# Performance work log

Hardware: AMD Instinct MI355X
Metric: run time of the kernel (lower is better)

Reference implementation:

```python
import jax, jax.numpy as jnp
import numpy as np

KV_SIZE = 512


def setup_inputs() -> dict:
    key = jax.random.key(0)
    k1, k2, k3 = jax.random.split(key, 3)
    B, T, C = 8, 4096, 1024
    x = jax.random.normal(k1, (B, T, C), dtype=jnp.float32)
    k_t_1 = jax.random.normal(k2, (B, KV_SIZE, C), dtype=jnp.float32)
    v_t_1 = jax.random.normal(k3, (B, KV_SIZE, C), dtype=jnp.float32)
    return {"x": x, "k_t_1": k_t_1, "v_t_1": v_t_1}


def reference(x, k_t_1, v_t_1):
    # x: [B, T, C]; latent state k_t_1, v_t_1: [B, S=512, C]
    B, T, C = x.shape
    scale = 1.0 / jnp.sqrt(jnp.asarray(C, dtype=x.dtype))

    # Read: queries (tokens) attend over the fixed-size latent KV state.
    scores = jnp.einsum("btc,bsc->bts", x, k_t_1) * scale      # [B, T, S]
    att = jnp.einsum("bts,bsc->btc", jax.nn.softmax(scores, axis=-1), v_t_1)

    # Update: each latent slot attends over the incoming tokens and
    # accumulates the summary into the state (fixed-size KV cache update).
    k_scores = jnp.einsum("bsc,btc->bst", k_t_1, x) * scale     # [B, S, T]
    k_t = k_t_1 + jnp.einsum("bst,btc->bsc", jax.nn.softmax(k_scores, axis=-1), x)
    v_scores = jnp.einsum("bsc,btc->bst", v_t_1, x) * scale     # [B, S, T]
    v_t = v_t_1 + jnp.einsum("bst,btc->bsc", jax.nn.softmax(v_scores, axis=-1), x)

    return att, k_t, v_t
```

## Files before the change

kernel.cpp:

```cpp
#include <hip/hip_runtime.h>
#include <hip/hip_bf16.h>

#define BB 8
#define TT 4096
#define CC 1024
#define SS 512

typedef __bf16 bf16x8 __attribute__((ext_vector_type(8)));
typedef float f32x4 __attribute__((ext_vector_type(4)));
typedef unsigned short u16x8 __attribute__((ext_vector_type(8)));

__device__ __forceinline__ float bf2f(unsigned short u) {
  union { unsigned int i; float f; } x; x.i = ((unsigned int)u) << 16; return x.f;
}
__device__ __forceinline__ unsigned short f2bf(float f) {
  __hip_bfloat16 h = __float2bfloat16(f);
  unsigned short u; __builtin_memcpy(&u, &h, 2); return u;
}

__global__ void cvt_transpose(const float* __restrict__ in,
                              unsigned short* __restrict__ out_rm,
                              unsigned short* __restrict__ out_t,
                              int R, int Cd) {
  __shared__ float tile[64][65];
  const long bo = (long)blockIdx.z * R * Cd;
  const int r0 = blockIdx.x * 64, c0 = blockIdx.y * 64;
  const int tx = threadIdx.x, ty = threadIdx.y;
#pragma unroll
  for (int i = 0; i < 16; ++i) {
    int r = ty + i * 4;
    float v = in[bo + (long)(r0 + r) * Cd + c0 + tx];
    tile[r][tx] = v;
    out_rm[bo + (long)(r0 + r) * Cd + c0 + tx] = f2bf(v);
  }
  if (out_t != nullptr) {
    __syncthreads();
#pragma unroll
    for (int i = 0; i < 16; ++i) {
      int c = ty + i * 4;
      out_t[bo + (long)(c0 + c) * R + r0 + tx] = f2bf(tile[tx][c]);
    }
  }
}

__global__ void transpose_bf16(const unsigned short* __restrict__ in,
                               unsigned short* __restrict__ out,
                               int Rin, int Cin) {
  __shared__ unsigned short tile[64][72];
  const long bo = (long)blockIdx.z * Rin * Cin;
  const int r0 = blockIdx.x * 64, c0 = blockIdx.y * 64;
  const int tid = threadIdx.x;
  const int lr = tid >> 3;
  const int lc = (tid & 7) * 8;
#pragma unroll
  for (int p = 0; p < 2; ++p) {
    int r = lr + p * 32;
    *(u16x8*)&tile[r][lc] = *(const u16x8*)&in[bo + (long)(r0 + r) * Cin + c0 + lc];
  }
  __syncthreads();
#pragma unroll
  for (int p = 0; p < 2; ++p) {
    int s = lr + p * 32;
    u16x8 val;
#pragma unroll
    for (int j = 0; j < 8; ++j) val[j] = tile[lc + j][s];
    *(u16x8*)&out[bo + (long)(c0 + s) * Rin + r0 + lc] = val;
  }
}

template <int ROWLEN>
__global__ __launch_bounds__(256) void row_softmax(unsigned short* __restrict__ sc) {
  constexpr int NV = ROWLEN / 512;
  const int lane = threadIdx.x & 63;
  const long row = (long)blockIdx.x * 4 + (threadIdx.x >> 6);
  unsigned short* base = sc + row * (long)ROWLEN;
  u16x8 d[NV];
  float m = -1e30f;
#pragma unroll
  for (int v = 0; v < NV; ++v) {
    d[v] = *(const u16x8*)&base[(v * 64 + lane) * 8];
#pragma unroll
    for (int j = 0; j < 8; ++j) m = fmaxf(m, bf2f(d[v][j]));
  }
#pragma unroll
  for (int off = 32; off >= 1; off >>= 1) m = fmaxf(m, __shfl_xor(m, off, 64));
  float l = 0.f;
#pragma unroll
  for (int v = 0; v < NV; ++v) {
#pragma unroll
    for (int j = 0; j < 8; ++j) {
      float e = __expf(bf2f(d[v][j]) - m);
      l += e;
      d[v][j] = f2bf(e);
    }
  }
#pragma unroll
  for (int off = 32; off >= 1; off >>= 1) l += __shfl_xor(l, off, 64);
  const float inv = 1.f / l;
#pragma unroll
  for (int v = 0; v < NV; ++v) {
    u16x8 o;
#pragma unroll
    for (int j = 0; j < 8; ++j) o[j] = f2bf(bf2f(d[v][j]) * inv);
    *(u16x8*)&base[(v * 64 + lane) * 8] = o;
  }
}

template <bool OUT_BF16, bool RESID>
__global__ __launch_bounds__(256) void gemm_bt(
    const unsigned short* __restrict__ A, int lda, long sA,
    const unsigned short* __restrict__ Bt, int ldb, long sB,
    void* __restrict__ Cout, int ldc, long sC,
    const float* __restrict__ resid, long sR,
    float alpha, int M, int N, int K) {
  __shared__ unsigned short As[128 * 64];
  __shared__ unsigned short Bs[128 * 64];
  const int zb = blockIdx.z;
  const unsigned short* Ab = A + (long)zb * sA;
  const unsigned short* Bb = Bt + (long)zb * sB;
  const int m0 = blockIdx.y * 128;
  const int n0 = blockIdx.x * 128;
  const int tid = threadIdx.x;
  const int lane = tid & 63;
  const int wm = (tid >> 6) & 1;
  const int wn = tid >> 7;
  const int srow = tid >> 3;
  const int scol = (tid & 7) * 8;
  f32x4 zero = {0.f, 0.f, 0.f, 0.f};
  f32x4 acc[4][4];
#pragma unroll
  for (int i = 0; i < 4; ++i)
#pragma unroll
    for (int j = 0; j < 4; ++j) acc[i][j] = zero;

  for (int k0 = 0; k0 < K; k0 += 64) {
#pragma unroll
    for (int p = 0; p < 4; ++p) {
      int r = srow + p * 32;
      const unsigned short* g = Ab + (long)(m0 + r) * lda + k0 + scol;
      __builtin_amdgcn_global_load_lds(
          (const __attribute__((address_space(1))) void*)g,
          (__attribute__((address_space(3))) void*)&As[r * 64 + scol], 16, 0, 0);
    }
#pragma unroll
    for (int p = 0; p < 4; ++p) {
      int r = srow + p * 32;
      const unsigned short* g = Bb + (long)(n0 + r) * ldb + k0 + scol;
      __builtin_amdgcn_global_load_lds(
          (const __attribute__((address_space(1))) void*)g,
          (__attribute__((address_space(3))) void*)&Bs[r * 64 + scol], 16, 0, 0);
    }
    __syncthreads();
#pragma unroll
    for (int kk = 0; kk < 2; ++kk) {
      const int kof = kk * 32 + (lane >> 4) * 8;
      bf16x8 af[4], bfr[4];
#pragma unroll
      for (int i = 0; i < 4; ++i)
        af[i] = *(const bf16x8*)&As[(wm * 64 + i * 16 + (lane & 15)) * 64 + kof];
#pragma unroll
      for (int j = 0; j < 4; ++j)
        bfr[j] = *(const bf16x8*)&Bs[(wn * 64 + j * 16 + (lane & 15)) * 64 + kof];
#pragma unroll
      for (int i = 0; i < 4; ++i)
#pragma unroll
        for (int j = 0; j < 4; ++j)
          acc[i][j] = __builtin_amdgcn_mfma_f32_16x16x32_bf16(af[i], bfr[j], acc[i][j], 0, 0, 0);
    }
    __syncthreads();
  }
  const int rbase = (lane >> 4) * 4;
  const int cl = lane & 15;
#pragma unroll
  for (int i = 0; i < 4; ++i)
#pragma unroll
    for (int j = 0; j < 4; ++j)
#pragma unroll
      for (int r = 0; r < 4; ++r) {
        int row = m0 + wm * 64 + i * 16 + rbase + r;
        int col = n0 + wn * 64 + j * 16 + cl;
        long idx = (long)row * ldc + col;
        float v = acc[i][j][r] * alpha;
        if (RESID) v += resid[(long)zb * sR + idx];
        if (OUT_BF16)
          ((unsigned short*)Cout)[(long)zb * sC + idx] = f2bf(v);
        else
          ((float*)Cout)[(long)zb * sC + idx] = v;
      }
}

extern "C" void kernel_launch(void* const* d_in, const int* in_sizes, int n_in,
                              void* d_out, int out_size, void* d_ws, size_t ws_size,
                              hipStream_t stream) {
  const float* x = (const float*)d_in[0];
  const float* kin = (const float*)d_in[1];
  const float* vin = (const float*)d_in[2];

  float* att = (float*)d_out;
  float* kt = att + (long)BB * TT * CC;
  float* vt = kt + (long)BB * SS * CC;

  unsigned short* xb = (unsigned short*)d_out;
  unsigned short* xT = xb + (long)BB * TT * CC;

  char* w = (char*)d_ws;
  unsigned short* kb = (unsigned short*)w; w += (long)BB * SS * CC * 2;
  unsigned short* vb = (unsigned short*)w; w += (long)BB * SS * CC * 2;
  unsigned short* vT = (unsigned short*)w; w += (long)BB * CC * SS * 2;
  unsigned short* sc = (unsigned short*)w; w += (long)BB * TT * SS * 2;
  unsigned short* pk = (unsigned short*)w; w += (long)BB * SS * TT * 2;

  const float scale = 0.03125f;
  dim3 cblk(64, 4);

  cvt_transpose<<<dim3(TT / 64, CC / 64, BB), cblk, 0, stream>>>(x, xb, xT, TT, CC);
  cvt_transpose<<<dim3(SS / 64, CC / 64, BB), cblk, 0, stream>>>(kin, kb, (unsigned short*)nullptr, SS, CC);
  cvt_transpose<<<dim3(SS / 64, CC / 64, BB), cblk, 0, stream>>>(vin, vb, vT, SS, CC);

  gemm_bt<true, false><<<dim3(SS / 128, TT / 128, BB), 256, 0, stream>>>(
      xb, CC, (long)TT * CC, kb, CC, (long)SS * CC, sc, SS, (long)TT * SS,
      nullptr, 0, scale, TT, SS, CC);

  transpose_bf16<<<dim3(TT / 64, SS / 64, BB), 256, 0, stream>>>(sc, pk, TT, SS);
  row_softmax<TT><<<BB * SS / 4, 256, 0, stream>>>(pk);

  gemm_bt<false, true><<<dim3(CC / 128, SS / 128, BB), 256, 0, stream>>>(
      pk, TT, (long)SS * TT, xT, TT, (long)CC * TT, kt, CC, (long)SS * CC,
      kin, (long)SS * CC, 1.f, SS, CC, TT);

  row_softmax<SS><<<BB * TT / 4, 256, 0, stream>>>(sc);

  gemm_bt<true, false><<<dim3(TT / 128, SS / 128, BB), 256, 0, stream>>>(
      vb, CC, (long)SS * CC, xb, CC, (long)TT * CC, pk, TT, (long)SS * TT,
      nullptr, 0, scale, SS, TT, CC);
  row_softmax<TT><<<BB * SS / 4, 256, 0, stream>>>(pk);

  gemm_bt<false, true><<<dim3(CC / 128, SS / 128, BB), 256, 0, stream>>>(
      pk, TT, (long)SS * TT, xT, TT, (long)CC * TT, vt, CC, (long)SS * CC,
      vin, (long)SS * CC, 1.f, SS, CC, TT);

  gemm_bt<false, false><<<dim3(CC / 128, TT / 128, BB), 256, 0, stream>>>(
      sc, SS, (long)TT * SS, vT, SS, (long)CC * SS, att, CC, (long)TT * CC,
      nullptr, 0, 1.f, TT, CC, SS);
}
```

Before: 717.3 us.

## Split-K the update GEMMs with atomics and batch the K/V score GEMMs

The P·x update GEMMs now split their long T reduction across extra blocks and accumulate with float atomics. The k_t/v_t outputs are pre-seeded with the fp32 inputs during conversion, so the residual add is folded in. When the workspace is large enough, the K and V score GEMMs run as one launch over stacked rows, and their softmaxes also run as one launch. The T×S score matrix for the read path is obtained by transposing the k·xᵀ scores instead of recomputing them. This targets under-occupancy of the 256-block update GEMMs, at the cost of atomic traffic, nondeterministic summation order, and workspace aliasing that depends on ws_size.

Result: faster. 700.2 us (-2.4%).

```diff
diff --git a/kernel.cpp b/kernel.cpp
--- a/kernel.cpp
+++ b/kernel.cpp
@@ -21,6 +21,7 @@
 __global__ void cvt_transpose(const float* __restrict__ in,
                               unsigned short* __restrict__ out_rm,
                               unsigned short* __restrict__ out_t,
+                              float* __restrict__ out_f32,
                               int R, int Cd) {
   __shared__ float tile[64][65];
   const long bo = (long)blockIdx.z * R * Cd;
@@ -32,6 +33,7 @@
     float v = in[bo + (long)(r0 + r) * Cd + c0 + tx];
     tile[r][tx] = v;
     out_rm[bo + (long)(r0 + r) * Cd + c0 + tx] = f2bf(v);
+    if (out_f32 != nullptr) out_f32[bo + (long)(r0 + r) * Cd + c0 + tx] = v;
   }
   if (out_t != nullptr) {
     __syncthreads();
@@ -45,9 +47,10 @@
 
 __global__ void transpose_bf16(const unsigned short* __restrict__ in,
                                unsigned short* __restrict__ out,
-                               int Rin, int Cin) {
+                               int Rin, int Cin, long sIn, long sOut) {
   __shared__ unsigned short tile[64][72];
-  const long bo = (long)blockIdx.z * Rin * Cin;
+  const long bi = (long)blockIdx.z * sIn;
+  const long bo = (long)blockIdx.z * sOut;
   const int r0 = blockIdx.x * 64, c0 = blockIdx.y * 64;
   const int tid = threadIdx.x;
   const int lr = tid >> 3;
@@ -55,7 +58,7 @@
 #pragma unroll
   for (int p = 0; p < 2; ++p) {
     int r = lr + p * 32;
-    *(u16x8*)&tile[r][lc] = *(const u16x8*)&in[bo + (long)(r0 + r) * Cin + c0 + lc];
+    *(u16x8*)&tile[r][lc] = *(const u16x8*)&in[bi + (long)(r0 + r) * Cin + c0 + lc];
   }
   __syncthreads();
 #pragma unroll
@@ -106,19 +109,27 @@
   }
 }
 
-template <bool OUT_BF16, bool RESID>
+template <bool OUT_BF16, bool ATOMIC>
 __global__ __launch_bounds__(256) void gemm_bt(
-    const unsigned short* __restrict__ A, int lda, long sA,
+    const unsigned short* __restrict__ A,
+    const unsigned short* __restrict__ A2, int lda, long sA,
     const unsigned short* __restrict__ Bt, int ldb, long sB,
-    void* __restrict__ Cout, int ldc, long sC,
-    const float* __restrict__ resid, long sR,
-    float alpha, int M, int N, int K) {
+    void* __restrict__ Cout, void* __restrict__ Cout2, int ldc, long sC,
+    float alpha, int M, int N, int K, int halfM, int kshift) {
   __shared__ unsigned short As[128 * 64];
   __shared__ unsigned short Bs[128 * 64];
-  const int zb = blockIdx.z;
-  const unsigned short* Ab = A + (long)zb * sA;
+  const int zb = blockIdx.z >> kshift;
+  const int kch = blockIdx.z & ((1 << kshift) - 1);
+  const int Kc = K >> kshift;
+  const int kstart = kch * Kc;
+  const int kend = kstart + Kc;
+  const int m0full = blockIdx.y * 128;
+  const bool hi = m0full >= halfM;
+  const unsigned short* Ab = ((hi && A2 != nullptr) ? A2 : A) + (long)zb * sA;
+  const int mA = (hi && A2 != nullptr) ? m0full - halfM : m0full;
+  void* Cbase = (hi && Cout2 != nullptr) ? Cout2 : Cout;
+  const int mC = (hi && Cout2 != nullptr) ? m0full - halfM : m0full;
   const unsigned short* Bb = Bt + (long)zb * sB;
-  const int m0 = blockIdx.y * 128;
   const int n0 = blockIdx.x * 128;
   const int tid = threadIdx.x;
   const int lane = tid & 63;
@@ -133,11 +144,11 @@
 #pragma unroll
     for (int j = 0; j < 4; ++j) acc[i][j] = zero;
 
-  for (int k0 = 0; k0 < K; k0 += 64) {
+  for (int k0 = kstart; k0 < kend; k0 += 64) {
 #pragma unroll
     for (int p = 0; p < 4; ++p) {
       int r = srow + p * 32;
-      const unsigned short* g = Ab + (long)(m0 + r) * lda + k0 + scol;
+      const unsigned short* g = Ab + (long)(mA + r) * lda + k0 + scol;
       __builtin_amdgcn_global_load_lds(
           (const __attribute__((address_space(1))) void*)g,
           (__attribute__((address_space(3))) void*)&As[r * 64 + scol], 16, 0, 0);
@@ -177,15 +188,17 @@
     for (int j = 0; j < 4; ++j)
 #pragma unroll
       for (int r = 0; r < 4; ++r) {
-        int row = m0 + wm * 64 + i * 16 + rbase + r;
+        int row = mC + wm * 64 + i * 16 + rbase + r;
         int col = n0 + wn * 64 + j * 16 + cl;
-        long idx = (long)row * ldc + col;
+        long idx = (long)zb * sC + (long)row * ldc + col;
         float v = acc[i][j][r] * alpha;
-        if (RESID) v += resid[(long)zb * sR + idx];
-        if (OUT_BF16)
-          ((unsigned short*)Cout)[(long)zb * sC + idx] = f2bf(v);
-        else
-          ((float*)Cout)[(long)zb * sC + idx] = v;
+        if (ATOMIC) {
+          unsafeAtomicAdd(&((float*)Cbase)[idx], v);
+        } else if (OUT_BF16) {
+          ((unsigned short*)Cbase)[idx] = f2bf(v);
+        } else {
+          ((float*)Cbase)[idx] = v;
+        }
       }
 }
 
@@ -203,43 +216,73 @@
   unsigned short* xb = (unsigned short*)d_out;
   unsigned short* xT = xb + (long)BB * TT * CC;
 
-  char* w = (char*)d_ws;
-  unsigned short* kb = (unsigned short*)w; w += (long)BB * SS * CC * 2;
-  unsigned short* vb = (unsigned short*)w; w += (long)BB * SS * CC * 2;
-  unsigned short* vT = (unsigned short*)w; w += (long)BB * CC * SS * 2;
-  unsigned short* sc = (unsigned short*)w; w += (long)BB * TT * SS * 2;
-  unsigned short* pk = (unsigned short*)w; w += (long)BB * SS * TT * 2;
-
   const float scale = 0.03125f;
   dim3 cblk(64, 4);
-
-  cvt_transpose<<<dim3(TT / 64, CC / 64, BB), cblk, 0, stream>>>(x, xb, xT, TT, CC);
-  cvt_transpose<<<dim3(SS / 64, CC / 64, BB), cblk, 0, stream>>>(kin, kb, (unsigned short*)nullptr, SS, CC);
-  cvt_transpose<<<dim3(SS / 64, CC / 64, BB), cblk, 0, stream>>>(vin, vb, vT, SS, CC);
-
-  gemm_bt<true, false><<<dim3(SS / 128, TT / 128, BB), 256, 0, stream>>>(
-      xb, CC, (long)TT * CC, kb, CC, (long)SS * CC, sc, SS, (long)TT * SS,
-      nullptr, 0, scale, TT, SS, CC);
-
-  transpose_bf16<<<dim3(TT / 64, SS / 64, BB), 256, 0, stream>>>(sc, pk, TT, SS);
-  row_softmax<TT><<<BB * SS / 4, 256, 0, stream>>>(pk);
-
-  gemm_bt<false, true><<<dim3(CC / 128, SS / 128, BB), 256, 0, stream>>>(
-      pk, TT, (long)SS * TT, xT, TT, (long)CC * TT, kt, CC, (long)SS * CC,
-      kin, (long)SS * CC, 1.f, SS, CC, TT);
-
-  row_softmax<SS><<<BB * TT / 4, 256, 0, stream>>>(sc);
-
-  gemm_bt<true, false><<<dim3(TT / 128, SS / 128, BB), 256, 0, stream>>>(
-      vb, CC, (long)SS * CC, xb, CC, (long)TT * CC, pk, TT, (long)SS * TT,
-      nullptr, 0, scale, SS, TT, CC);
-  row_softmax<TT><<<BB * SS / 4, 256, 0, stream>>>(pk);
-
-  gemm_bt<false, true><<<dim3(CC / 128, SS / 128, BB), 256, 0, stream>>>(
-      pk, TT, (long)SS * TT, xT, TT, (long)CC * TT, vt, CC, (long)SS * CC,
-      vin, (long)SS * CC, 1.f, SS, CC, TT);
-
-  gemm_bt<false, false><<<dim3(CC / 128, TT / 128, BB), 256, 0, stream>>>(
-      sc, SS, (long)TT * SS, vT, SS, (long)CC * SS, att, CC, (long)TT * CC,
-      nullptr, 0, 1.f, TT, CC, SS);
-}
+  const long MiB = 1024 * 1024;
+
+  if (ws_size >= (size_t)(104 * MiB)) {
+    char* w = (char*)d_ws;
+    unsigned short* sc  = (unsigned short*)w;
+    unsigned short* kb  = (unsigned short*)w;
+    unsigned short* vb  = (unsigned short*)(w + 8 * MiB);
+    unsigned short* vT  = (unsigned short*)(w + 32 * MiB);
+    unsigned short* pkv = (unsigned short*)(w + 40 * MiB);
+
+    cvt_transpose<<<dim3(TT / 64, CC / 64, BB), cblk, 0, stream>>>(x, xb, xT, nullptr, TT, CC);
+    cvt_transpose<<<dim3(SS / 64, CC / 64, BB), cblk, 0, stream>>>(kin, kb, nullptr, kt, SS, CC);
+    cvt_transpose<<<dim3(SS / 64, CC / 64, BB), cblk, 0, stream>>>(vin, vb, vT, vt, SS, CC);
+
+    gemm_bt<true, false><<<dim3(TT / 128, 2 * SS / 128, BB), 256, 0, stream>>>(
+        kb, vb, CC, (long)SS * CC, xb, CC, (long)TT * CC,
+        pkv, nullptr, TT, (long)2 * SS * TT, scale, 2 * SS, TT, CC, SS, 0);
+
+    transpose_bf16<<<dim3(SS / 64, TT / 64, BB), 256, 0, stream>>>(
+        pkv, sc, SS, TT, (long)2 * SS * TT, (long)TT * SS);
+
+    row_softmax<TT><<<BB * 2 * SS / 4, 256, 0, stream>>>(pkv);
+
+    gemm_bt<false, true><<<dim3(CC / 128, 2 * SS / 128, BB * 2), 256, 0, stream>>>(
+        pkv, nullptr, TT, (long)2 * SS * TT, xT, TT, (long)CC * TT,
+        kt, vt, CC, (long)SS * CC, 1.f, 2 * SS, CC, TT, SS, 1);
+
+    row_softmax<SS><<<BB * TT / 4, 256, 0, stream>>>(sc);
+
+    gemm_bt<false, false><<<dim3(CC / 128, TT / 128, BB), 256, 0, stream>>>(
+        sc, nullptr, SS, (long)TT * SS, vT, SS, (long)CC * SS,
+        att, nullptr, CC, (long)TT * CC, 1.f, TT, CC, SS, 1 << 30, 0);
+  } else {
+    char* w = (char*)d_ws;
+    unsigned short* kb = (unsigned short*)w;
+    unsigned short* vb = (unsigned short*)(w + 8 * MiB);
+    unsigned short* vT = (unsigned short*)(w + 16 * MiB);
+    unsigned short* sc = (unsigned short*)(w + 24 * MiB);
+    unsigned short* pk = (unsigned short*)(w + 56 * MiB);
+
+    cvt_transpose<<<dim3(TT / 64, CC / 64, BB), cblk, 0, stream>>>(x, xb, xT, nullptr, TT, CC);
+    cvt_transpose<<<dim3(SS / 64, CC / 64, BB), cblk, 0, stream>>>(kin, kb, nullptr, kt, SS, CC);
+    cvt_transpose<<<dim3(SS / 64, CC / 64, BB), cblk, 0, stream>>>(vin, vb, vT, vt, SS, CC);
+
+    gemm_bt<true, false><<<dim3(TT / 128, SS / 128, BB), 256, 0, stream>>>(
+        kb, nullptr, CC, (long)SS * CC, xb, CC, (long)TT * CC,
+        pk, nullptr, TT, (long)SS * TT, scale, SS, TT, CC, 1 << 30, 0);
+    transpose_bf16<<<dim3(SS / 64, TT / 64, BB), 256, 0, stream>>>(
+        pk, sc, SS, TT, (long)SS * TT, (long)TT * SS);
+    row_softmax<TT><<<BB * SS / 4, 256, 0, stream>>>(pk);
+    gemm_bt<false, true><<<dim3(CC / 128, SS / 128, BB * 4), 256, 0, stream>>>(
+        pk, nullptr, TT, (long)SS * TT, xT, TT, (long)CC * TT,
+        kt, nullptr, CC, (long)SS * CC, 1.f, SS, CC, TT, 1 << 30, 2);
+
+    gemm_bt<true, false><<<dim3(TT / 128, SS / 128, BB), 256, 0, stream>>>(
+        vb, nullptr, CC, (long)SS * CC, xb, CC, (long)TT * CC,
+        pk, nullptr, TT, (long)SS * TT, scale, SS, TT, CC, 1 << 30, 0);
+    row_softmax<TT><<<BB * SS / 4, 256, 0, stream>>>(pk);
+    gemm_bt<false, true><<<dim3(CC / 128, SS / 128, BB * 4), 256, 0, stream>>>(
+        pk, nullptr, TT, (long)SS * TT, xT, TT, (long)CC * TT,
+        vt, nullptr, CC, (long)SS * CC, 1.f, SS, CC, TT, 1 << 30, 2);
+
+    row_softmax<SS><<<BB * TT / 4, 256, 0, stream>>>(sc);
+    gemm_bt<false, false><<<dim3(CC / 128, TT / 128, BB), 256, 0, stream>>>(
+        sc, nullptr, SS, (long)TT * SS, vT, SS, (long)CC * SS,
+        att, nullptr, CC, (long)TT * CC, 1.f, TT, CC, SS, 1 << 30, 0);
+  }
+}
```
